# Performance work log

Measured on AMD Instinct MI355X. Metric: run time of the kernel, lower is better.

## Reference

```python
import jax, jax.numpy as jnp
import numpy as np

D_MODEL = 256
N_HEAD = 8
D_FF = 2048
B, N = 8, 1024
NEG = -9e15
EPS = 1e-5


def _layernorm(x, g, b):
    mu = jnp.mean(x, axis=-1, keepdims=True)
    var = jnp.mean(jnp.square(x - mu), axis=-1, keepdims=True)
    return (x - mu) * jax.lax.rsqrt(var + EPS) * g + b


def setup_inputs() -> dict:
    key = jax.random.key(0)
    ks = jax.random.split(key, 12)
    d, dff = D_MODEL, D_FF
    s = 1.0 / np.sqrt(d)
    inp = {
        "src": jax.random.normal(ks[0], (B, N, d), dtype=jnp.float32),
        "adj": jax.random.randint(ks[1], (B, N, N), 0, 2, dtype=jnp.int32),
        "W_gat": jax.random.normal(ks[2], (d, d), dtype=jnp.float32) * s,
        "a_gat": jax.random.normal(ks[3], (2 * d, 1), dtype=jnp.float32) * s,
        "in_proj_w": jax.random.normal(ks[4], (3 * d, d), dtype=jnp.float32) * s,
        "in_proj_b": jnp.zeros((3 * d,), dtype=jnp.float32),
        "out_proj_w": jax.random.normal(ks[5], (d, d), dtype=jnp.float32) * s,
        "out_proj_b": jnp.zeros((d,), dtype=jnp.float32),
        "lin1_w": jax.random.normal(ks[6], (dff, d), dtype=jnp.float32) * s,
        "lin1_b": jnp.zeros((dff,), dtype=jnp.float32),
        "lin2_w": jax.random.normal(ks[7], (d, dff), dtype=jnp.float32) * (1.0 / np.sqrt(dff)),
        "lin2_b": jnp.zeros((d,), dtype=jnp.float32),
        "ln1_g": jnp.ones((d,), dtype=jnp.float32),
        "ln1_b": jnp.zeros((d,), dtype=jnp.float32),
        "ln2_g": jnp.ones((d,), dtype=jnp.float32),
        "ln2_b": jnp.zeros((d,), dtype=jnp.float32),
        "ln3_g": jnp.ones((d,), dtype=jnp.float32),
        "ln3_b": jnp.zeros((d,), dtype=jnp.float32),
    }
    return inp


def reference(src, adj, W_gat, a_gat, in_proj_w, in_proj_b, out_proj_w, out_proj_b,
              lin1_w, lin1_b, lin2_w, lin2_b, ln1_g, ln1_b, ln2_g, ln2_b, ln3_g, ln3_b):
    d = D_MODEL
    # --- Graph attention (dropout inactive in eval) ---
    Wh = jnp.matmul(src, W_gat)                      # [B,N,d]
    a1 = a_gat[:d, 0]
    a2 = a_gat[d:, 0]
    # e[b,i,j] = Wh_i . a1 + Wh_j . a2  (equivalent to concat+matmul in source)
    f1 = Wh @ a1                                     # [B,N]
    f2 = Wh @ a2                                     # [B,N]
    e = f1[:, :, None] + f2[:, None, :]              # [B,N,N]
    e = jnp.where(adj > 0, e, NEG)
    attn = jax.nn.softmax(e, axis=-1)
    h_prime = jnp.matmul(attn, Wh)                   # [B,N,d]
    graph_out = jax.nn.elu(h_prime)
    x = _layernorm(src + graph_out, ln1_g, ln1_b)

    # --- Multi-head self-attention ---
    qkv = x @ in_proj_w.T + in_proj_b                # [B,N,3d]
    q, k, v = jnp.split(qkv, 3, axis=-1)
    hd = d // N_HEAD
    def heads(t):
        return t.reshape(B, N, N_HEAD, hd).transpose(0, 2, 1, 3)  # [B,H,N,hd]
    q, k, v = heads(q), heads(k), heads(v)
    scores = jnp.einsum("bhid,bhjd->bhij", q, k) / np.sqrt(hd)
    probs = jax.nn.softmax(scores, axis=-1)
    ctx = jnp.einsum("bhij,bhjd->bhid", probs, v)
    ctx = ctx.transpose(0, 2, 1, 3).reshape(B, N, d)
    attn_out = ctx @ out_proj_w.T + out_proj_b
    y = _layernorm(x + attn_out, ln2_g, ln2_b)

    # --- FFN ---
    ff = jax.nn.relu(y @ lin1_w.T + lin1_b) @ lin2_w.T + lin2_b
    return _layernorm(y + ff, ln3_g, ln3_b)
```

## Files before the change

### kernel.cpp

```cpp
#include <hip/hip_runtime.h>
#include <math.h>

constexpr int BATCH = 8;
constexpr int SEQ   = 1024;
constexpr int DM    = 256;
constexpr int DF    = 2048;
constexpr int NH    = 8;
constexpr int HDIM  = 32;
constexpr int ROWS  = BATCH * SEQ;
constexpr float NEGV = -9e15f;
constexpr float EPSV = 1e-5f;
constexpr float QSCALE = 0.2550351822f;
constexpr float LOG2E  = 1.44269504f;

typedef __attribute__((ext_vector_type(8))) short short8;
typedef __attribute__((ext_vector_type(4))) float f32x4;

static __device__ __forceinline__ ushort f2bf(float f) {
    unsigned x = __float_as_uint(f);
    unsigned r = (x + 0x7fffu + ((x >> 16) & 1u)) >> 16;
    return (ushort)r;
}
static __device__ __forceinline__ float bf2f(ushort u) {
    return __uint_as_float((unsigned)u << 16);
}
static __device__ __forceinline__ unsigned cvt_pk_bf16(float lo, float hi) {
    unsigned r;
    asm volatile("v_cvt_pk_bf16_f32 %0, %1, %2" : "=v"(r) : "v"(lo), "v"(hi));
    return r;
}

struct CastArgs {
    const float* in[5];
    ushort* out[5];
    int n4[5];
};
constexpr int CAST_BLKS = (2097152 + 196608 + 65536 + 524288 + 524288) / 4 / 256;

__global__ __launch_bounds__(256) void prep_k(CastArgs a,
                                              const float* __restrict__ W_gat,
                                              const float* __restrict__ a_gat,
                                              ushort* __restrict__ wgTb,
                                              float* __restrict__ w1,
                                              float* __restrict__ w2)
{
    __shared__ float Ts[32][33];
    const int bid = blockIdx.x;
    const int t = threadIdx.x;

    if (bid < CAST_BLKS) {
        int idx = bid * 256 + t;
        #pragma unroll
        for (int r = 0; r < 5; r++) {
            if (idx < a.n4[r]) {
                float4 v = *(const float4*)&a.in[r][(size_t)idx * 4];
                ushort4 o; o.x = f2bf(v.x); o.y = f2bf(v.y); o.z = f2bf(v.z); o.w = f2bf(v.w);
                *(ushort4*)&a.out[r][(size_t)idx * 4] = o;
                return;
            }
            idx -= a.n4[r];
        }
    } else if (bid < CAST_BLKS + 64) {
        const int bb = bid - CAST_BLKS;
        const int r0 = (bb >> 3) * 32, c0 = (bb & 7) * 32;
        const int lr = t >> 3, lc4 = (t & 7) * 4;
        float4 v = *(const float4*)&W_gat[(size_t)(r0 + lr) * DM + c0 + lc4];
        Ts[lr][lc4] = v.x; Ts[lr][lc4 + 1] = v.y; Ts[lr][lc4 + 2] = v.z; Ts[lr][lc4 + 3] = v.w;
        __syncthreads();
        const int oc = t >> 3, or4 = (t & 7) * 4;
        ushort4 o;
        o.x = f2bf(Ts[or4 + 0][oc]); o.y = f2bf(Ts[or4 + 1][oc]);
        o.z = f2bf(Ts[or4 + 2][oc]); o.w = f2bf(Ts[or4 + 3][oc]);
        *(ushort4*)&wgTb[(size_t)(c0 + oc) * DM + r0 + or4] = o;
    } else {
        const int k = (bid - CAST_BLKS - 64) * 4 + (t >> 6);
        const int l = t & 63;
        float4 wv = *(const float4*)&W_gat[(size_t)k * DM + 4 * l];
        float4 a1 = *(const float4*)&a_gat[4 * l];
        float4 a2 = *(const float4*)&a_gat[DM + 4 * l];
        float s1 = wv.x*a1.x + wv.y*a1.y + wv.z*a1.z + wv.w*a1.w;
        float s2 = wv.x*a2.x + wv.y*a2.y + wv.z*a2.z + wv.w*a2.w;
        #pragma unroll
        for (int off = 32; off; off >>= 1) {
            s1 += __shfl_xor(s1, off, 64);
            s2 += __shfl_xor(s2, off, 64);
        }
        if (l == 0) { w1[k] = s1; w2[k] = s2; }
    }
}

__global__ __launch_bounds__(256) void f12_k(const float* __restrict__ src,
                                             const float* __restrict__ w1,
                                             const float* __restrict__ w2,
                                             float* __restrict__ f1,
                                             float* __restrict__ f2)
{
    const size_t row = (size_t)blockIdx.x * 4 + (threadIdx.x >> 6);
    const int l = threadIdx.x & 63;
    float4 sv = *(const float4*)&src[row * DM + 4 * l];
    float4 v1 = *(const float4*)&w1[4 * l];
    float4 v2 = *(const float4*)&w2[4 * l];
    float s1 = sv.x*v1.x + sv.y*v1.y + sv.z*v1.z + sv.w*v1.w;
    float s2 = sv.x*v2.x + sv.y*v2.y + sv.z*v2.z + sv.w*v2.w;
    #pragma unroll
    for (int off = 32; off; off >>= 1) {
        s1 += __shfl_xor(s1, off, 64);
        s2 += __shfl_xor(s2, off, 64);
    }
    if (l == 0) { f1[row] = s1 * LOG2E; f2[row] = s2 * LOG2E; }
}

template<int EP, int BM, int BN>
__global__ __launch_bounds__(256) void gemm_bf(const ushort* __restrict__ A,
                                               const ushort* __restrict__ B,
                                               const float* __restrict__ bias,
                                               ushort* __restrict__ Cb,
                                               int N, int K, int ldB,
                                               long long sA, long long sB, long long sC)
{
    __shared__ ushort As[2][BM][40];
    __shared__ ushort Bs[2][BN][40];
    A += (size_t)blockIdx.z * sA;
    B += (size_t)blockIdx.z * sB;

    const int t  = threadIdx.x;
    const int m0 = blockIdx.y * BM, n0 = blockIdx.x * BN;
    const int lane = t & 63, lo = lane & 15, hi = lane >> 4;
    const int w = t >> 6;
    constexpr int NI = BM / 32, NJ = BN / 32;
    const int wr = (w >> 1) * (BM / 2);
    const int wc = (w & 1) * (BN / 2);

    const int lrA = (BM == 128) ? (t >> 1) : (t >> 2);
    const int lcA = (BM == 128) ? ((t & 1) * 16) : ((t & 3) * 8);
    const int lrB = (BN == 128) ? (t >> 1) : (t >> 2);
    const int lcB = (BN == 128) ? ((t & 1) * 16) : ((t & 3) * 8);

    f32x4 acc[NI][NJ];
    const f32x4 zero = {0.f, 0.f, 0.f, 0.f};
    #pragma unroll
    for (int i = 0; i < NI; i++)
        #pragma unroll
        for (int j = 0; j < NJ; j++) acc[i][j] = zero;

    const ushort* Ap = A + (size_t)(m0 + lrA) * K + lcA;
    const ushort* Bp = B + (size_t)(n0 + lrB) * ldB + lcB;

    short8 ar0, ar1, br0, br1;
    ar0 = *(const short8*)(Ap);
    if constexpr (BM == 128) ar1 = *(const short8*)(Ap + 8);
    br0 = *(const short8*)(Bp);
    if constexpr (BN == 128) br1 = *(const short8*)(Bp + 8);
    *(short8*)&As[0][lrA][lcA] = ar0;
    if constexpr (BM == 128) *(short8*)&As[0][lrA][lcA + 8] = ar1;
    *(short8*)&Bs[0][lrB][lcB] = br0;
    if constexpr (BN == 128) *(short8*)&Bs[0][lrB][lcB + 8] = br1;

    const int NT = K >> 5;
    for (int it = 0; it < NT; it++) {
        const int cur = it & 1;
        if (it + 1 < NT) {
            const int k0 = (it + 1) << 5;
            ar0 = *(const short8*)(Ap + k0);
            if constexpr (BM == 128) ar1 = *(const short8*)(Ap + k0 + 8);
            br0 = *(const short8*)(Bp + k0);
            if constexpr (BN == 128) br1 = *(const short8*)(Bp + k0 + 8);
        }
        __syncthreads();

        short8 afr[NI], bfr[NJ];
        #pragma unroll
        for (int i = 0; i < NI; i++) afr[i] = *(const short8*)&As[cur][wr + i*16 + lo][hi * 8];
        #pragma unroll
        for (int j = 0; j < NJ; j++) bfr[j] = *(const short8*)&Bs[cur][wc + j*16 + lo][hi * 8];
        #pragma unroll
        for (int i = 0; i < NI; i++)
            #pragma unroll
            for (int j = 0; j < NJ; j++)
                acc[i][j] = __builtin_amdgcn_mfma_f32_16x16x32_bf16(afr[i], bfr[j], acc[i][j], 0, 0, 0);

        if (it + 1 < NT) {
            *(short8*)&As[cur ^ 1][lrA][lcA] = ar0;
            if constexpr (BM == 128) *(short8*)&As[cur ^ 1][lrA][lcA + 8] = ar1;
            *(short8*)&Bs[cur ^ 1][lrB][lcB] = br0;
            if constexpr (BN == 128) *(short8*)&Bs[cur ^ 1][lrB][lcB + 8] = br1;
        }
    }

    Cb += (size_t)blockIdx.z * sC;
    #pragma unroll
    for (int j = 0; j < NJ; j++) {
        const int col = n0 + wc + j * 16 + lo;
        float bj = (EP == 1 || EP == 2 || EP == 6) ? bias[col] : 0.f;
        #pragma unroll
        for (int i = 0; i < NI; i++) {
            const int rbase = m0 + wr + i * 16 + hi * 4;
            #pragma unroll
            for (int r = 0; r < 4; r++) {
                float v = acc[i][j][r] + bj;
                if (EP == 3) v = v > 0.f ? v : expm1f(v);
                if (EP == 2) v = fmaxf(v, 0.f);
                if (EP == 6 && col < DM) v *= QSCALE;
                Cb[(size_t)(rbase + r) * N + col] = f2bf(v);
            }
        }
    }
}

template<bool WB>
__global__ __launch_bounds__(256) void ln_k(const float* __restrict__ a,
                                            const ushort* __restrict__ r,
                                            const float* __restrict__ g,
                                            const float* __restrict__ be,
                                            float* __restrict__ o,
                                            ushort* __restrict__ ob)
{
    const size_t row = (size_t)blockIdx.x * 4 + (threadIdx.x >> 6);
    const int l = threadIdx.x & 63;
    float4 av = *(const float4*)&a[row * DM + 4 * l];
    ushort4 rv = *(const ushort4*)&r[row * DM + 4 * l];
    float v0 = av.x + bf2f(rv.x);
    float v1 = av.y + bf2f(rv.y);
    float v2 = av.z + bf2f(rv.z);
    float v3 = av.w + bf2f(rv.w);
    float s = (v0 + v1) + (v2 + v3);
    #pragma unroll
    for (int off = 32; off; off >>= 1) s += __shfl_xor(s, off, 64);
    const float mu = s * (1.0f / DM);
    float q = (v0-mu)*(v0-mu) + (v1-mu)*(v1-mu) + (v2-mu)*(v2-mu) + (v3-mu)*(v3-mu);
    #pragma unroll
    for (int off = 32; off; off >>= 1) q += __shfl_xor(q, off, 64);
    const float rs = rsqrtf(q * (1.0f / DM) + EPSV);
    float4 gv = *(const float4*)&g[4 * l];
    float4 bv = *(const float4*)&be[4 * l];
    float4 ov;
    ov.x = (v0 - mu) * rs * gv.x + bv.x;
    ov.y = (v1 - mu) * rs * gv.y + bv.y;
    ov.z = (v2 - mu) * rs * gv.z + bv.z;
    ov.w = (v3 - mu) * rs * gv.w + bv.w;
    *(float4*)&o[row * DM + 4 * l] = ov;
    if (WB) {
        ushort4 obv;
        obv.x = f2bf(ov.x); obv.y = f2bf(ov.y); obv.z = f2bf(ov.z); obv.w = f2bf(ov.w);
        *(ushort4*)&ob[row * DM + 4 * l] = obv;
    }
}

__global__ __launch_bounds__(256) void gat_sm_k(const int* __restrict__ adj,
                                                const float* __restrict__ f1,
                                                const float* __restrict__ f2,
                                                ushort* __restrict__ P)
{
    const int row = blockIdx.x * 4 + (threadIdx.x >> 6);
    const int b = row >> 10;
    const int l = threadIdx.x & 63;
    const int* arow = adj + (size_t)row * SEQ;
    const float* f2b = f2 + ((size_t)b << 10);
    const float f1i = f1[row];

    float e[16];
    float mx = -3.4e38f;
    #pragma unroll
    for (int u = 0; u < 4; u++) {
        const int j = 4 * l + 256 * u;
        int4 a4 = *(const int4*)&arow[j];
        float4 f4 = *(const float4*)&f2b[j];
        e[4*u+0] = a4.x > 0 ? f1i + f4.x : NEGV;
        e[4*u+1] = a4.y > 0 ? f1i + f4.y : NEGV;
        e[4*u+2] = a4.z > 0 ? f1i + f4.z : NEGV;
        e[4*u+3] = a4.w > 0 ? f1i + f4.w : NEGV;
        mx = fmaxf(mx, fmaxf(fmaxf(e[4*u], e[4*u+1]), fmaxf(e[4*u+2], e[4*u+3])));
    }
    #pragma unroll
    for (int off = 32; off; off >>= 1) mx = fmaxf(mx, __shfl_xor(mx, off, 64));
    float s = 0.f;
    #pragma unroll
    for (int k = 0; k < 16; k++) { e[k] = exp2f(e[k] - mx); s += e[k]; }
    #pragma unroll
    for (int off = 32; off; off >>= 1) s += __shfl_xor(s, off, 64);
    const float inv = 1.0f / s;
    #pragma unroll
    for (int u = 0; u < 4; u++) {
        ushort4 o;
        o.x = f2bf(e[4*u+0] * inv); o.y = f2bf(e[4*u+1] * inv);
        o.z = f2bf(e[4*u+2] * inv); o.w = f2bf(e[4*u+3] * inv);
        *(ushort4*)&P[(size_t)row * SEQ + 4 * l + 256 * u] = o;
    }
}

__device__ __forceinline__ int vt_idx(int d, int kv) { return d * 72 + ((d >> 3) & 3) * 16 + kv; }
constexpr int VTSZ = 32 * 72 + 3 * 16 + 8;

__global__ __launch_bounds__(256) void mha_k(const ushort* __restrict__ qkv,
                                             ushort* __restrict__ ctxb)
{
    __shared__ ushort Ks[2][64][40];
    __shared__ ushort Vt[2][VTSZ];
    __shared__ ushort Ps[64][72];

    const int blk = blockIdx.x;
    const int grp = blk & 63, qt = blk >> 6;
    const int h = grp & 7, b = grp >> 3;
    const int i0 = qt << 6;
    const int t = threadIdx.x;
    const int w = t >> 6, lane = t & 63, lo = lane & 15, hi = lane >> 4;
    const int gsh = lane & 48;
    const size_t base = (size_t)b * SEQ * 768;

    const short8 aQ = *(const short8*)(qkv + base + (size_t)(i0 + 16*w + lo) * 768 + h * HDIM + hi * 8);
    short8 ones;
    #pragma unroll
    for (int e = 0; e < 8; e++) ones[e] = (short)0x3F80;

    const int srow = t >> 2, scb = (t & 3) << 3;
    const int vcol = (srow & 32) | ((srow & 15) << 1) | ((srow >> 4) & 1);
    {
        const ushort* p0 = qkv + base + (size_t)srow * 768 + h * HDIM;
        short8 k0 = *(const short8*)(p0 + 256 + scb);
        short8 v0 = *(const short8*)(p0 + 512 + scb);
        *(short8*)&Ks[0][srow][scb] = k0;
        #pragma unroll
        for (int e = 0; e < 8; e++) Vt[0][vt_idx(scb + e, vcol)] = (ushort)v0[e];
    }

    float m_run[4], l_run[4];
    f32x4 O0 = {0.f, 0.f, 0.f, 0.f}, O1 = {0.f, 0.f, 0.f, 0.f};
    #pragma unroll
    for (int r = 0; r < 4; r++) { m_run[r] = -3.0e38f; l_run[r] = 0.f; }
    const f32x4 zero = {0.f, 0.f, 0.f, 0.f};

    short8 kreg, vreg;
    for (int it = 0; it < 16; it++) {
        const int cur = it & 1;
        if (it < 15) {
            const ushort* nb = qkv + base + (size_t)((it + 1) * 64 + srow) * 768 + h * HDIM;
            kreg = *(const short8*)(nb + 256 + scb);
            vreg = *(const short8*)(nb + 512 + scb);
        }
        __syncthreads();

        f32x4 S[4];
        #pragma unroll
        for (int jt = 0; jt < 4; jt++) {
            short8 bK = *(const short8*)&Ks[cur][16 * jt + lo][hi * 8];
            S[jt] = __builtin_amdgcn_mfma_f32_16x16x32_bf16(aQ, bK, zero, 0, 0, 0);
        }

        float mxl[4];
        bool any = false;
        #pragma unroll
        for (int r = 0; r < 4; r++) {
            mxl[r] = fmaxf(fmaxf(S[0][r], S[1][r]), fmaxf(S[2][r], S[3][r]));
            any = any || (mxl[r] > m_run[r] + 8.f);
        }
        unsigned long long bal = __ballot(any);
        if ((bal >> gsh) & 0xffffULL) {
            #pragma unroll
            for (int r = 0; r < 4; r++) {
                float mx = mxl[r];
                #pragma unroll
                for (int off = 8; off; off >>= 1) mx = fmaxf(mx, __shfl_xor(mx, off, 16));
                float mnew = fmaxf(m_run[r], mx);
                float sc = exp2f(m_run[r] - mnew);
                m_run[r] = mnew;
                l_run[r] *= sc; O0[r] *= sc; O1[r] *= sc;
            }
        }
        #pragma unroll
        for (int r = 0; r < 4; r++) {
            const int row = 16 * w + 4 * hi + r;
            unsigned u01 = cvt_pk_bf16(exp2f(S[0][r] - m_run[r]), exp2f(S[1][r] - m_run[r]));
            unsigned u23 = cvt_pk_bf16(exp2f(S[2][r] - m_run[r]), exp2f(S[3][r] - m_run[r]));
            *(unsigned*)&Ps[row][2 * lo]      = u01;
            *(unsigned*)&Ps[row][32 + 2 * lo] = u23;
        }

        f32x4 O2 = zero;
        #pragma unroll
        for (int kt = 0; kt < 2; kt++) {
            short8 aP  = *(const short8*)&Ps[16 * w + lo][32 * kt + hi * 8];
            short8 bV0 = *(const short8*)&Vt[cur][vt_idx(lo,      32 * kt + hi * 8)];
            short8 bV1 = *(const short8*)&Vt[cur][vt_idx(16 + lo, 32 * kt + hi * 8)];
            O0 = __builtin_amdgcn_mfma_f32_16x16x32_bf16(aP, bV0, O0, 0, 0, 0);
            O1 = __builtin_amdgcn_mfma_f32_16x16x32_bf16(aP, bV1, O1, 0, 0, 0);
            O2 = __builtin_amdgcn_mfma_f32_16x16x32_bf16(aP, ones, O2, 0, 0, 0);
        }
        #pragma unroll
        for (int r = 0; r < 4; r++) l_run[r] += O2[r];

        if (it < 15) {
            *(short8*)&Ks[cur ^ 1][srow][scb] = kreg;
            #pragma unroll
            for (int e = 0; e < 8; e++) Vt[cur ^ 1][vt_idx(scb + e, vcol)] = (ushort)vreg[e];
        }
    }

    #pragma unroll
    for (int r = 0; r < 4; r++) {
        float inv = 1.0f / l_run[r];
        size_t row = (size_t)b * SEQ + i0 + 16 * w + 4 * hi + r;
        ctxb[row * DM + h * HDIM + lo]      = f2bf(O0[r] * inv);
        ctxb[row * DM + h * HDIM + 16 + lo] = f2bf(O1[r] * inv);
    }
}

extern "C" void kernel_launch(void* const* d_in, const int* in_sizes, int n_in,
                              void* d_out, int out_size, void* d_ws, size_t ws_size,
                              hipStream_t stream)
{
    const float* src        = (const float*)d_in[0];
    const int*   adj        = (const int*)  d_in[1];
    const float* W_gat      = (const float*)d_in[2];
    const float* a_gat      = (const float*)d_in[3];
    const float* in_proj_w  = (const float*)d_in[4];
    const float* in_proj_b  = (const float*)d_in[5];
    const float* out_proj_w = (const float*)d_in[6];
    const float* out_proj_b = (const float*)d_in[7];
    const float* lin1_w     = (const float*)d_in[8];
    const float* lin1_b     = (const float*)d_in[9];
    const float* lin2_w     = (const float*)d_in[10];
    const float* lin2_b     = (const float*)d_in[11];
    const float* ln1_g      = (const float*)d_in[12];
    const float* ln1_b_     = (const float*)d_in[13];
    const float* ln2_g      = (const float*)d_in[14];
    const float* ln2_b_     = (const float*)d_in[15];
    const float* ln3_g      = (const float*)d_in[16];
    const float* ln3_b_     = (const float*)d_in[17];

    char* base = (char*)d_ws;
    const size_t MB = 1024 * 1024;
    ushort* tmpb  = (ushort*)(base + 0 * MB);
    float*  x     = (float*) (base + 4 * MB);
    float*  y     = (float*) (base + 12 * MB);
    ushort* P_bf  = (ushort*)(base + 20 * MB);
    ushort* qkvb  = (ushort*)(base + 20 * MB);
    ushort* ff1b  = (ushort*)(base + 20 * MB);
    ushort* srcb  = (ushort*)(base + 52 * MB);
    ushort* WhTb  = (ushort*)(base + 56 * MB);
    ushort* xb    = (ushort*)(base + 60 * MB);
    ushort* yb    = (ushort*)(base + 64 * MB);
    ushort* ctxb  = (ushort*)(base + 68 * MB);
    float*  f1    = (float*) (base + 72 * MB);
    float*  f2    = f1 + ROWS;
    float*  w1    = f2 + ROWS;
    float*  w2    = w1 + DM;
    ushort* wgTb  = (ushort*)(base + 73 * MB);
    ushort* ipwb  = wgTb + 65536;
    ushort* opwb  = ipwb + 196608;
    ushort* l1wb  = opwb + 65536;
    ushort* l2wb  = l1wb + 524288;

    dim3 b256(256);

    CastArgs ca;
    ca.in[0] = src;       ca.out[0] = srcb; ca.n4[0] = 2097152 / 4;
    ca.in[1] = in_proj_w; ca.out[1] = ipwb; ca.n4[1] = 196608 / 4;
    ca.in[2] = out_proj_w;ca.out[2] = opwb; ca.n4[2] = 65536 / 4;
    ca.in[3] = lin1_w;    ca.out[3] = l1wb; ca.n4[3] = 524288 / 4;
    ca.in[4] = lin2_w;    ca.out[4] = l2wb; ca.n4[4] = 524288 / 4;
    prep_k<<<CAST_BLKS + 64 + 64, b256, 0, stream>>>(ca, W_gat, a_gat, wgTb, w1, w2);

    f12_k<<<ROWS / 4, b256, 0, stream>>>(src, w1, w2, f1, f2);
    gemm_bf<5, 64, 64><<<dim3(ROWS/64, DM/64, 1), b256, 0, stream>>>(wgTb, srcb, nullptr, WhTb,
                                                                     ROWS, DM, DM, 0, 0, 0);
    gat_sm_k<<<ROWS / 4, b256, 0, stream>>>(adj, f1, f2, P_bf);
    gemm_bf<3, 64, 64><<<dim3(DM/64, SEQ/64, 8), b256, 0, stream>>>(P_bf, WhTb, nullptr, tmpb,
                                                                    DM, SEQ, ROWS,
                                                                    (long long)SEQ * SEQ, (long long)SEQ, (long long)SEQ * DM);
    ln_k<true><<<ROWS / 4, b256, 0, stream>>>(src, tmpb, ln1_g, ln1_b_, x, xb);

    gemm_bf<6, 128, 64><<<dim3(768/64, ROWS/128, 1), b256, 0, stream>>>(xb, ipwb, in_proj_b, qkvb,
                                                                        768, DM, DM, 0, 0, 0);
    mha_k<<<BATCH * NH * (SEQ / 64), b256, 0, stream>>>(qkvb, ctxb);
    gemm_bf<1, 64, 64><<<dim3(DM/64, ROWS/64, 1), b256, 0, stream>>>(ctxb, opwb, out_proj_b, tmpb,
                                                                     DM, DM, DM, 0, 0, 0);
    ln_k<true><<<ROWS / 4, b256, 0, stream>>>(x, tmpb, ln2_g, ln2_b_, y, yb);

    gemm_bf<2, 128, 128><<<dim3(DF/128, ROWS/128, 1), b256, 0, stream>>>(yb, l1wb, lin1_b, ff1b,
                                                                         DF, DM, DM, 0, 0, 0);
    gemm_bf<1, 64, 64><<<dim3(DM/64, ROWS/64, 1), b256, 0, stream>>>(ff1b, l2wb, lin2_b, tmpb,
                                                                     DM, DF, DF, 0, 0, 0);
    ln_k<false><<<ROWS / 4, b256, 0, stream>>>(y, tmpb, ln3_g, ln3_b_, (float*)d_out, nullptr);
}
```

Baseline: 156.4 us.

## Drop fp32 residual copies and double MHA query tile per block

The layernorm kernels now read the residual from the bf16 copy instead of a separate fp32 buffer, and the fp32 x/y outputs are no longer written. This cuts residual memory traffic at the cost of bf16 rounding in the residual path. The attention kernel now uses 512 threads per block covering 128 queries, with K and V staging split across the two thread halves, so each K/V tile is shared by more query rows. That halves the K/V global reads but increases per-block shared memory and register pressure.

```diff
diff --git a/kernel.cpp b/kernel.cpp
--- a/kernel.cpp
+++ b/kernel.cpp
@@ -207,22 +207,28 @@
     }
 }
 
-template<bool WB>
-__global__ __launch_bounds__(256) void ln_k(const float* __restrict__ a,
+template<int MODE>
+__global__ __launch_bounds__(256) void ln_k(const float* __restrict__ af,
+                                            const ushort* __restrict__ ab,
                                             const ushort* __restrict__ r,
                                             const float* __restrict__ g,
                                             const float* __restrict__ be,
-                                            float* __restrict__ o,
+                                            float* __restrict__ of,
                                             ushort* __restrict__ ob)
 {
     const size_t row = (size_t)blockIdx.x * 4 + (threadIdx.x >> 6);
     const int l = threadIdx.x & 63;
-    float4 av = *(const float4*)&a[row * DM + 4 * l];
     ushort4 rv = *(const ushort4*)&r[row * DM + 4 * l];
-    float v0 = av.x + bf2f(rv.x);
-    float v1 = av.y + bf2f(rv.y);
-    float v2 = av.z + bf2f(rv.z);
-    float v3 = av.w + bf2f(rv.w);
+    float v0, v1, v2, v3;
+    if (MODE == 0) {
+        float4 av = *(const float4*)&af[row * DM + 4 * l];
+        v0 = av.x + bf2f(rv.x); v1 = av.y + bf2f(rv.y);
+        v2 = av.z + bf2f(rv.z); v3 = av.w + bf2f(rv.w);
+    } else {
+        ushort4 av = *(const ushort4*)&ab[row * DM + 4 * l];
+        v0 = bf2f(av.x) + bf2f(rv.x); v1 = bf2f(av.y) + bf2f(rv.y);
+        v2 = bf2f(av.z) + bf2f(rv.z); v3 = bf2f(av.w) + bf2f(rv.w);
+    }
     float s = (v0 + v1) + (v2 + v3);
     #pragma unroll
     for (int off = 32; off; off >>= 1) s += __shfl_xor(s, off, 64);
@@ -233,15 +239,16 @@
     const float rs = rsqrtf(q * (1.0f / DM) + EPSV);
     float4 gv = *(const float4*)&g[4 * l];
     float4 bv = *(const float4*)&be[4 * l];
-    float4 ov;
-    ov.x = (v0 - mu) * rs * gv.x + bv.x;
-    ov.y = (v1 - mu) * rs * gv.y + bv.y;
-    ov.z = (v2 - mu) * rs * gv.z + bv.z;
-    ov.w = (v3 - mu) * rs * gv.w + bv.w;
-    *(float4*)&o[row * DM + 4 * l] = ov;
-    if (WB) {
+    float o0 = (v0 - mu) * rs * gv.x + bv.x;
+    float o1 = (v1 - mu) * rs * gv.y + bv.y;
+    float o2 = (v2 - mu) * rs * gv.z + bv.z;
+    float o3 = (v3 - mu) * rs * gv.w + bv.w;
+    if (MODE == 2) {
+        float4 ov; ov.x = o0; ov.y = o1; ov.z = o2; ov.w = o3;
+        *(float4*)&of[row * DM + 4 * l] = ov;
+    } else {
         ushort4 obv;
-        obv.x = f2bf(ov.x); obv.y = f2bf(ov.y); obv.z = f2bf(ov.z); obv.w = f2bf(ov.w);
+        obv.x = f2bf(o0); obv.y = f2bf(o1); obv.z = f2bf(o2); obv.w = f2bf(o3);
         *(ushort4*)&ob[row * DM + 4 * l] = obv;
     }
 }
@@ -291,17 +298,17 @@
 __device__ __forceinline__ int vt_idx(int d, int kv) { return d * 72 + ((d >> 3) & 3) * 16 + kv; }
 constexpr int VTSZ = 32 * 72 + 3 * 16 + 8;
 
-__global__ __launch_bounds__(256) void mha_k(const ushort* __restrict__ qkv,
+__global__ __launch_bounds__(512) void mha_k(const ushort* __restrict__ qkv,
                                              ushort* __restrict__ ctxb)
 {
     __shared__ ushort Ks[2][64][40];
     __shared__ ushort Vt[2][VTSZ];
-    __shared__ ushort Ps[64][72];
+    __shared__ ushort Ps[128][72];
 
     const int blk = blockIdx.x;
     const int grp = blk & 63, qt = blk >> 6;
     const int h = grp & 7, b = grp >> 3;
-    const int i0 = qt << 6;
+    const int i0 = qt << 7;
     const int t = threadIdx.x;
     const int w = t >> 6, lane = t & 63, lo = lane & 15, hi = lane >> 4;
     const int gsh = lane & 48;
@@ -312,15 +319,18 @@
     #pragma unroll
     for (int e = 0; e < 8; e++) ones[e] = (short)0x3F80;
 
-    const int srow = t >> 2, scb = (t & 3) << 3;
+    const int tt = t & 255;
+    const int srow = tt >> 2, scb = (tt & 3) << 3;
+    const bool isK = t < 256;
     const int vcol = (srow & 32) | ((srow & 15) << 1) | ((srow >> 4) & 1);
     {
-        const ushort* p0 = qkv + base + (size_t)srow * 768 + h * HDIM;
-        short8 k0 = *(const short8*)(p0 + 256 + scb);
-        short8 v0 = *(const short8*)(p0 + 512 + scb);
-        *(short8*)&Ks[0][srow][scb] = k0;
-        #pragma unroll
-        for (int e = 0; e < 8; e++) Vt[0][vt_idx(scb + e, vcol)] = (ushort)v0[e];
+        const ushort* p0 = qkv + base + (size_t)srow * 768 + h * HDIM + (isK ? 256 : 512) + scb;
+        short8 v0 = *(const short8*)p0;
+        if (isK) *(short8*)&Ks[0][srow][scb] = v0;
+        else {
+            #pragma unroll
+            for (int e = 0; e < 8; e++) Vt[0][vt_idx(scb + e, vcol)] = (ushort)v0[e];
+        }
     }
 
     float m_run[4], l_run[4];
@@ -329,14 +339,12 @@
     for (int r = 0; r < 4; r++) { m_run[r] = -3.0e38f; l_run[r] = 0.f; }
     const f32x4 zero = {0.f, 0.f, 0.f, 0.f};
 
-    short8 kreg, vreg;
+    short8 reg;
     for (int it = 0; it < 16; it++) {
         const int cur = it & 1;
-        if (it < 15) {
-            const ushort* nb = qkv + base + (size_t)((it + 1) * 64 + srow) * 768 + h * HDIM;
-            kreg = *(const short8*)(nb + 256 + scb);
-            vreg = *(const short8*)(nb + 512 + scb);
-        }
+        if (it < 15)
+            reg = *(const short8*)(qkv + base + (size_t)((it + 1) * 64 + srow) * 768
+                                   + h * HDIM + (isK ? 256 : 512) + scb);
         __syncthreads();
 
         f32x4 S[4];
@@ -389,9 +397,11 @@
         for (int r = 0; r < 4; r++) l_run[r] += O2[r];
 
         if (it < 15) {
-            *(short8*)&Ks[cur ^ 1][srow][scb] = kreg;
-            #pragma unroll
-            for (int e = 0; e < 8; e++) Vt[cur ^ 1][vt_idx(scb + e, vcol)] = (ushort)vreg[e];
+            if (isK) *(short8*)&Ks[cur ^ 1][srow][scb] = reg;
+            else {
+                #pragma unroll
+                for (int e = 0; e < 8; e++) Vt[cur ^ 1][vt_idx(scb + e, vcol)] = (ushort)reg[e];
+            }
         }
     }
 
@@ -430,21 +440,19 @@
     char* base = (char*)d_ws;
     const size_t MB = 1024 * 1024;
     ushort* tmpb  = (ushort*)(base + 0 * MB);
-    float*  x     = (float*) (base + 4 * MB);
-    float*  y     = (float*) (base + 12 * MB);
-    ushort* P_bf  = (ushort*)(base + 20 * MB);
-    ushort* qkvb  = (ushort*)(base + 20 * MB);
-    ushort* ff1b  = (ushort*)(base + 20 * MB);
-    ushort* srcb  = (ushort*)(base + 52 * MB);
-    ushort* WhTb  = (ushort*)(base + 56 * MB);
-    ushort* xb    = (ushort*)(base + 60 * MB);
-    ushort* yb    = (ushort*)(base + 64 * MB);
-    ushort* ctxb  = (ushort*)(base + 68 * MB);
-    float*  f1    = (float*) (base + 72 * MB);
+    ushort* P_bf  = (ushort*)(base + 4 * MB);
+    ushort* qkvb  = (ushort*)(base + 4 * MB);
+    ushort* ff1b  = (ushort*)(base + 4 * MB);
+    ushort* srcb  = (ushort*)(base + 36 * MB);
+    ushort* WhTb  = (ushort*)(base + 40 * MB);
+    ushort* xb    = (ushort*)(base + 44 * MB);
+    ushort* yb    = (ushort*)(base + 48 * MB);
+    ushort* ctxb  = (ushort*)(base + 52 * MB);
+    float*  f1    = (float*) (base + 56 * MB);
     float*  f2    = f1 + ROWS;
     float*  w1    = f2 + ROWS;
     float*  w2    = w1 + DM;
-    ushort* wgTb  = (ushort*)(base + 73 * MB);
+    ushort* wgTb  = (ushort*)(base + 57 * MB);
     ushort* ipwb  = wgTb + 65536;
     ushort* opwb  = ipwb + 196608;
     ushort* l1wb  = opwb + 65536;
@@ -467,18 +475,18 @@
     gemm_bf<3, 64, 64><<<dim3(DM/64, SEQ/64, 8), b256, 0, stream>>>(P_bf, WhTb, nullptr, tmpb,
                                                                     DM, SEQ, ROWS,
                                                                     (long long)SEQ * SEQ, (long long)SEQ, (long long)SEQ * DM);
-    ln_k<true><<<ROWS / 4, b256, 0, stream>>>(src, tmpb, ln1_g, ln1_b_, x, xb);
+    ln_k<0><<<ROWS / 4, b256, 0, stream>>>(src, nullptr, tmpb, ln1_g, ln1_b_, nullptr, xb);
 
     gemm_bf<6, 128, 64><<<dim3(768/64, ROWS/128, 1), b256, 0, stream>>>(xb, ipwb, in_proj_b, qkvb,
                                                                         768, DM, DM, 0, 0, 0);
-    mha_k<<<BATCH * NH * (SEQ / 64), b256, 0, stream>>>(qkvb, ctxb);
+    mha_k<<<BATCH * NH * (SEQ / 128), dim3(512), 0, stream>>>(qkvb, ctxb);
     gemm_bf<1, 64, 64><<<dim3(DM/64, ROWS/64, 1), b256, 0, stream>>>(ctxb, opwb, out_proj_b, tmpb,
                                                                      DM, DM, DM, 0, 0, 0);
-    ln_k<true><<<ROWS / 4, b256, 0, stream>>>(x, tmpb, ln2_g, ln2_b_, y, yb);
+    ln_k<1><<<ROWS / 4, b256, 0, stream>>>(nullptr, xb, tmpb, ln2_g, ln2_b_, nullptr, yb);
 
     gemm_bf<2, 128, 128><<<dim3(DF/128, ROWS/128, 1), b256, 0, stream>>>(yb, l1wb, lin1_b, ff1b,
                                                                          DF, DM, DM, 0, 0, 0);
     gemm_bf<1, 64, 64><<<dim3(DM/64, ROWS/64, 1), b256, 0, stream>>>(ff1b, l2wb, lin2_b, tmpb,
                                                                      DM, DF, DF, 0, 0, 0);
-    ln_k<false><<<ROWS / 4, b256, 0, stream>>>(y, tmpb, ln3_g, ln3_b_, (float*)d_out, nullptr);
-}
+    ln_k<2><<<ROWS / 4, b256, 0, stream>>>(nullptr, yb, tmpb, ln3_g, ln3_b_, (float*)d_out, nullptr);
+}
```

After: 155.8 us (median of 2 runs). Within noise of the previous version (-0.3%).
